# Optimization experiments

Measured on AMD Instinct MI355X. Metric: run time of the kernel, lower is better.

## Reference

```python
import jax, jax.numpy as jnp
import numpy as np

B, C, NMAX = 256, 1, 256   # graphs, channels, max nodes per graph
N = B * C * NMAX           # total nodes = 65536
E = N * 16                 # edges = 1,048,576
EMB, HID = 128, 128


def setup_inputs() -> dict:
    key = jax.random.key(0)
    ks = jax.random.split(key, 8)
    adj = jax.random.uniform(ks[0], (B, C, NMAX, NMAX), jnp.float32)
    edges = jax.random.randint(ks[1], (E, 2), 0, N, dtype=jnp.int32)
    subgraph_idx = jnp.repeat(jnp.arange(B, dtype=jnp.int32), C * NMAX)
    def lin(k, fan_in, fan_out):
        return jax.random.normal(k, (fan_in, fan_out), jnp.float32) / np.sqrt(fan_in).astype(np.float32)
    return {
        "adj": adj, "edges": edges, "subgraph_idx": subgraph_idx,
        "Wdec": lin(ks[2], NMAX, EMB), "bdec": jnp.zeros((EMB,), jnp.float32),
        "Wc1": lin(ks[3], EMB, HID),   "bc1": jnp.zeros((HID,), jnp.float32),
        "Wc2": lin(ks[4], HID, HID),   "bc2": jnp.zeros((HID,), jnp.float32),
        "Wp1": lin(ks[5], HID, HID),   "bp1": jnp.zeros((HID,), jnp.float32),
        "Wp2": lin(ks[6], HID, 1),     "bp2": jnp.zeros((1,), jnp.float32),
    }


def gcn_conv(x, W, b, src, dst):
    # PyG GCNConv: h = x W; add self-loops; symmetric normalization D^-1/2 (A+I) D^-1/2; + bias
    h = x @ W                                      # [N, out]
    deg = jnp.zeros((N,), x.dtype).at[dst].add(1.0) + 1.0  # in-degree incl. self loop
    dinv = jax.lax.rsqrt(deg)                      # [N]
    coef = dinv[src] * dinv[dst]                   # [E]
    agg = jax.ops.segment_sum(h[src] * coef[:, None], dst, num_segments=N)
    return agg + h * (dinv * dinv)[:, None] + b    # self-loop term + bias


def reference(adj, edges, subgraph_idx, Wdec, bdec, Wc1, bc1, Wc2, bc2, Wp1, bp1, Wp2, bp2):
    src, dst = edges[:, 0], edges[:, 1]
    # decoder_input: Linear(max_num_nodes -> embedding_dim) on flattened adjacency rows
    x = adj.reshape(-1, NMAX) @ Wdec + bdec        # [N, EMB]
    # forward applies convs[:-1] only (2 of the 3 convs); dropout is identity in eval mode
    x = jax.nn.relu(gcn_conv(x, Wc1, bc1, src, dst))
    x = jax.nn.relu(gcn_conv(x, Wc2, bc2, src, dst))
    # global max pool over nodes of each graph
    pooled = jax.ops.segment_max(x, subgraph_idx, num_segments=B)  # [B, HID]
    # post_mp MLP head
    h = jax.nn.relu(pooled @ Wp1 + bp1)
    return h @ Wp2 + bp2                           # [B, 1]
```

## Files before the change

### kernel.cpp

```cpp
#include <hip/hip_runtime.h>
#include <hip/hip_fp16.h>
#include <cstdint>
#include <cstddef>

#define NN   65536
#define NE   1048576
#define FD   128
#define KDEC 256
#define NGRAPH 256
#define DUMMY_SRC 65536u
#define EPB  4096
#define BCAP 4608
#define BCAPP 8448

typedef __attribute__((ext_vector_type(8))) short s16x8;
typedef __attribute__((ext_vector_type(4))) float f32x4;

__device__ __forceinline__ ushort f2bf(float x) {
  uint u = __float_as_uint(x);
  uint r = (u + 0x7fffu + ((u >> 16) & 1u)) >> 16;
  return (ushort)r;
}
__device__ __forceinline__ float bf2f(ushort h) {
  return __uint_as_float(((uint)h) << 16);
}

__device__ __forceinline__ void wsplit(float w, int k, int c,
                                       ushort* __restrict__ H,
                                       ushort* __restrict__ L) {
  ushort h = f2bf(w);
  size_t dst = ((size_t)((k >> 5) * 8 + (c >> 4)) * 64 +
                (size_t)((c & 15) + 16 * ((k & 31) >> 3))) * 8 + (k & 7);
  H[dst] = h;
  L[dst] = f2bf(w - bf2f(h));
}


__global__ __launch_bounds__(1024) void k_histbin(const int* __restrict__ edges,
                                                  uint* __restrict__ binbuf,
                                                  int* __restrict__ gbin,
                                                  const float* __restrict__ Wdec,
                                                  const float* __restrict__ Wc1,
                                                  const float* __restrict__ bdec,
                                                  float* __restrict__ bfused,
                                                  ushort* __restrict__ wfh,
                                                  ushort* __restrict__ wfl,
                                                  const float* __restrict__ Wc2,
                                                  ushort* __restrict__ w2h,
                                                  ushort* __restrict__ w2l) {
  const int b = blockIdx.x, t = threadIdx.x;
  if (b >= 256) {
    if (b < 288) {
      int i = (b - 256) * 1024 + t;
      int k = i >> 7, c = i & 127;
      float acc = 0.f;
#pragma unroll 8
      for (int j = 0; j < 128; j++) acc = fmaf(Wdec[k * FD + j], Wc1[j * FD + c], acc);
      wsplit(acc, k, c, wfh, wfl);
      if (b == 256 && t < 128) {
        float ba = 0.f;
        for (int j = 0; j < 128; j++) ba = fmaf(bdec[j], Wc1[j * FD + t], ba);
        bfused[t] = ba;
      }
    } else {
      int i = (b - 288) * 1024 + t;
      wsplit(Wc2[i], i >> 7, i & 127, w2h, w2l);
    }
    return;
  }
  __shared__ int lcnt[256];
  __shared__ int lsum[256];
  __shared__ int gbase[256];
  __shared__ uint sorted[EPB];

  if (t < 256) lcnt[t] = 0;
  __syncthreads();

  uint rec[4];
  ushort bkt[4], lidx[4];
#pragma unroll
  for (int r = 0; r < 4; r++) {
    int i = b * EPB + r * 1024 + t;
    int2 e = ((const int2*)edges)[i];
    int bucket = e.y >> 8;
    int li = atomicAdd(&lcnt[bucket], 1);
    rec[r] = ((uint)bucket << 24) | ((uint)(e.y & 255) << 16) | (uint)e.x;
    bkt[r] = (ushort)bucket;
    lidx[r] = (ushort)li;
  }
  __syncthreads();

  if (t < 256) lsum[t] = lcnt[t];
  __syncthreads();
  for (int off = 1; off < 256; off <<= 1) {
    int v = 0;
    if (t < 256 && t >= off) v = lsum[t - off];
    __syncthreads();
    if (t < 256) lsum[t] += v;
    __syncthreads();
  }
  if (t < 256) gbase[t] = atomicAdd(&gbin[t], lcnt[t]);
  __syncthreads();

#pragma unroll
  for (int r = 0; r < 4; r++) {
    int B = bkt[r];
    sorted[lsum[B] - lcnt[B] + lidx[r]] = rec[r];
  }
  __syncthreads();

  for (int s = t; s < EPB; s += 1024) {
    uint v = sorted[s];
    int B = v >> 24;
    int ex = lsum[B] - lcnt[B];
    binbuf[B * BCAP + gbase[B] + (s - ex)] = v & 0xFFFFFFu;
  }
}


__global__ __launch_bounds__(256) void k_misc(const uint* __restrict__ binbuf,
                                              const int* __restrict__ gbin,
                                              int* __restrict__ hist,
                                              int* __restrict__ offs,
                                              float* __restrict__ dinv,
                                              uint* __restrict__ ec) {
  __shared__ int lc[256];
  __shared__ int s[256];
  __shared__ int sofs[256];
  __shared__ int cnt2[256];
  const int b = blockIdx.x, t = threadIdx.x;
  lc[t] = 0;
  cnt2[t] = 0;
  __syncthreads();
  const int m = gbin[b];
  const uint* bp_ = binbuf + (size_t)b * BCAP;
  for (int i = t; i < m; i += 256)
    atomicAdd(&lc[bp_[i] >> 16], 1);
  __syncthreads();
  const int v = lc[t];
  const int vp = (v + 15) & ~15;
  s[t] = vp;
  __syncthreads();
  for (int off = 1; off < 256; off <<= 1) {
    int add = (t >= off) ? s[t - off] : 0;
    __syncthreads();
    s[t] += add;
    __syncthreads();
  }
  const int of = b * BCAPP + s[t] - vp;
  offs[b * 256 + t] = of;
  hist[b * 256 + t] = v;
  dinv[b * 256 + t] = rsqrtf((float)(v + 1));
  sofs[t] = of;
  __syncthreads();

  for (int i = t; i < m; i += 256) {
    uint rec = bp_[i];
    int dlow = rec >> 16;
    int pos = sofs[dlow] + atomicAdd(&cnt2[dlow], 1);
    ec[pos] = rec & 0xFFFFu;
  }
  __syncthreads();
  int base = sofs[t];
  for (int j = v; j < vp; j++) ec[base + j] = DUMMY_SRC;
}


template <bool ASPLIT>
__global__ __launch_bounds__(256) void k_gemm(const void* __restrict__ A0,
                                              const void* __restrict__ A1,
                                              const ushort* __restrict__ Whi,
                                              const ushort* __restrict__ Wlo,
                                              const float* __restrict__ bias,
                                              const float* __restrict__ scale,
                                              ushort* __restrict__ Y, int K) {
  __shared__ ushort Bs[2][8192];
  const int t = threadIdx.x;
  const int w = t >> 6;
  const int l = t & 63;
  const int lr = l & 15;
  const int kg = l >> 4;
  const int r0 = blockIdx.x * 128 + w * 32;
  const int nks = K >> 5;

  f32x4 acc[2][8];
#pragma unroll
  for (int mb = 0; mb < 2; mb++)
#pragma unroll
    for (int nb = 0; nb < 8; nb++) acc[mb][nb] = (f32x4)0.f;

  f32x4 araw[4];
  s16x8 ahn[2], aln[2];
  s16x8 bh0, bh1, bl0, bl1;

  auto issueA = [&](int s) {
#pragma unroll
    for (int mb = 0; mb < 2; mb++) {
      size_t base = (size_t)(r0 + mb * 16 + lr) * K + s * 32 + kg * 8;
      if (ASPLIT) {
        ahn[mb] = *(const s16x8*)((const ushort*)A0 + base);
        aln[mb] = *(const s16x8*)((const ushort*)A1 + base);
      } else {
        const float* xp = (const float*)A0 + base;
        araw[mb * 2] = *(const f32x4*)xp;
        araw[mb * 2 + 1] = *(const f32x4*)(xp + 4);
      }
    }
  };
  auto issueB = [&](int s) {
    const ushort* ph = Whi + (size_t)s * 4096 + t * 16;
    const ushort* pl = Wlo + (size_t)s * 4096 + t * 16;
    bh0 = *(const s16x8*)ph;
    bh1 = *(const s16x8*)(ph + 8);
    bl0 = *(const s16x8*)pl;
    bl1 = *(const s16x8*)(pl + 8);
  };
  auto writeB = [&](int buf) {
    *(s16x8*)&Bs[buf][t * 16] = bh0;
    *(s16x8*)&Bs[buf][t * 16 + 8] = bh1;
    *(s16x8*)&Bs[buf][4096 + t * 16] = bl0;
    *(s16x8*)&Bs[buf][4096 + t * 16 + 8] = bl1;
  };

  issueB(0);
  issueA(0);
  writeB(0);
  __syncthreads();

  int buf = 0;
  for (int s = 0; s < nks; ++s) {
    s16x8 ah[2], al[2];
    if (ASPLIT) {
      ah[0] = ahn[0]; ah[1] = ahn[1];
      al[0] = aln[0]; al[1] = aln[1];
    } else {
#pragma unroll
      for (int mb = 0; mb < 2; mb++) {
        float xv[8] = {araw[mb*2].x, araw[mb*2].y, araw[mb*2].z, araw[mb*2].w,
                       araw[mb*2+1].x, araw[mb*2+1].y, araw[mb*2+1].z, araw[mb*2+1].w};
        union { ushort u[8]; s16x8 v; } H, L;
#pragma unroll
        for (int e = 0; e < 8; e++) {
          ushort h = f2bf(xv[e]);
          H.u[e] = h;
          L.u[e] = f2bf(xv[e] - bf2f(h));
        }
        ah[mb] = H.v;
        al[mb] = L.v;
      }
    }
    const bool more = (s + 1 < nks);
    if (more) { issueB(s + 1); issueA(s + 1); }

#pragma unroll
    for (int nb = 0; nb < 8; nb++) {
      s16x8 bh = *(const s16x8*)&Bs[buf][nb * 512 + l * 8];
      s16x8 bl = *(const s16x8*)&Bs[buf][4096 + nb * 512 + l * 8];
#pragma unroll
      for (int mb = 0; mb < 2; mb++) {
        acc[mb][nb] = __builtin_amdgcn_mfma_f32_16x16x32_bf16(ah[mb], bh, acc[mb][nb], 0, 0, 0);
        acc[mb][nb] = __builtin_amdgcn_mfma_f32_16x16x32_bf16(ah[mb], bl, acc[mb][nb], 0, 0, 0);
        acc[mb][nb] = __builtin_amdgcn_mfma_f32_16x16x32_bf16(al[mb], bh, acc[mb][nb], 0, 0, 0);
      }
    }
    if (more) {
      writeB(buf ^ 1);
      __syncthreads();
      buf ^= 1;
    }
  }

  float dvr[2][4];
#pragma unroll
  for (int mb = 0; mb < 2; mb++)
#pragma unroll
    for (int r = 0; r < 4; r++)
      dvr[mb][r] = scale ? scale[r0 + mb * 16 + kg * 4 + r] : 1.f;

#pragma unroll
  for (int nb = 0; nb < 8; nb++) {
    int col = nb * 16 + lr;
    float bv = bias ? bias[col] : 0.f;
#pragma unroll
    for (int mb = 0; mb < 2; mb++)
#pragma unroll
      for (int r = 0; r < 4; r++) {
        size_t row = (size_t)(r0 + mb * 16 + kg * 4 + r);
        Y[row * FD + col] = f2bf((acc[mb][nb][r] + bv) * dvr[mb][r]);
      }
  }
}


template <int EMIT>
__global__ __launch_bounds__(256) void k_agg(const ushort* __restrict__ h16,
                                             const uint* __restrict__ ec,
                                             const int* __restrict__ offs,
                                             const int* __restrict__ hist,
                                             const float* __restrict__ dinv,
                                             const float* __restrict__ bias,
                                             ushort* __restrict__ yhi,
                                             ushort* __restrict__ ylo,
                                             float* __restrict__ pooled) {
  __shared__ int pmax[128];
  const int t = threadIdx.x;
  if (EMIT == 1) {
    if (t < 128) pmax[t] = 0;
    __syncthreads();
  }
  const int n = blockIdx.x * 4 + (t >> 6);
  const int l = t & 63;
  const int half = l >> 5;
  const int dl = (l & 31) * 4;

  const int cnt_p = (hist[n] + 15) & ~15;
  const uint* ep = ec + offs[n];

  float a0 = 0.f, a1 = 0.f, a2 = 0.f, a3 = 0.f;
  float b0 = 0.f, b1 = 0.f, b2 = 0.f, b3 = 0.f;
  for (int i = half; i < cnt_p; i += 16) {
    uint s0 = ep[i];
    uint s1 = ep[i + 2];
    uint s2 = ep[i + 4];
    uint s3 = ep[i + 6];
    uint s4 = ep[i + 8];
    uint s5 = ep[i + 10];
    uint s6 = ep[i + 12];
    uint s7 = ep[i + 14];
    ushort4 v0 = *(const ushort4*)(h16 + ((size_t)s0 << 7) + dl);
    ushort4 v1 = *(const ushort4*)(h16 + ((size_t)s1 << 7) + dl);
    ushort4 v2 = *(const ushort4*)(h16 + ((size_t)s2 << 7) + dl);
    ushort4 v3 = *(const ushort4*)(h16 + ((size_t)s3 << 7) + dl);
    ushort4 v4 = *(const ushort4*)(h16 + ((size_t)s4 << 7) + dl);
    ushort4 v5 = *(const ushort4*)(h16 + ((size_t)s5 << 7) + dl);
    ushort4 v6 = *(const ushort4*)(h16 + ((size_t)s6 << 7) + dl);
    ushort4 v7 = *(const ushort4*)(h16 + ((size_t)s7 << 7) + dl);
    a0 += bf2f(v0.x); a1 += bf2f(v0.y); a2 += bf2f(v0.z); a3 += bf2f(v0.w);
    b0 += bf2f(v1.x); b1 += bf2f(v1.y); b2 += bf2f(v1.z); b3 += bf2f(v1.w);
    a0 += bf2f(v2.x); a1 += bf2f(v2.y); a2 += bf2f(v2.z); a3 += bf2f(v2.w);
    b0 += bf2f(v3.x); b1 += bf2f(v3.y); b2 += bf2f(v3.z); b3 += bf2f(v3.w);
    a0 += bf2f(v4.x); a1 += bf2f(v4.y); a2 += bf2f(v4.z); a3 += bf2f(v4.w);
    b0 += bf2f(v5.x); b1 += bf2f(v5.y); b2 += bf2f(v5.z); b3 += bf2f(v5.w);
    a0 += bf2f(v6.x); a1 += bf2f(v6.y); a2 += bf2f(v6.z); a3 += bf2f(v6.w);
    b0 += bf2f(v7.x); b1 += bf2f(v7.y); b2 += bf2f(v7.z); b3 += bf2f(v7.w);
  }
  a0 += b0; a1 += b1; a2 += b2; a3 += b3;
  a0 += __shfl_xor(a0, 32);
  a1 += __shfl_xor(a1, 32);
  a2 += __shfl_xor(a2, 32);
  a3 += __shfl_xor(a3, 32);

  if (l < 32) {
    float dv = dinv[n];
    ushort4 vs = *(const ushort4*)(h16 + ((size_t)n << 7) + dl);
    float4 bb = *(const float4*)(bias + dl);
    float o0 = fmaxf(fmaf(dv, a0 + bf2f(vs.x), bb.x), 0.f);
    float o1 = fmaxf(fmaf(dv, a1 + bf2f(vs.y), bb.y), 0.f);
    float o2 = fmaxf(fmaf(dv, a2 + bf2f(vs.z), bb.z), 0.f);
    float o3 = fmaxf(fmaf(dv, a3 + bf2f(vs.w), bb.w), 0.f);
    if (EMIT == 0) {
      ushort4 hi, lo;
      hi.x = f2bf(o0); lo.x = f2bf(o0 - bf2f(hi.x));
      hi.y = f2bf(o1); lo.y = f2bf(o1 - bf2f(hi.y));
      hi.z = f2bf(o2); lo.z = f2bf(o2 - bf2f(hi.z));
      hi.w = f2bf(o3); lo.w = f2bf(o3 - bf2f(hi.w));
      size_t base = (size_t)n * FD + dl;
      *(ushort4*)(yhi + base) = hi;
      *(ushort4*)(ylo + base) = lo;
    } else {
      atomicMax(&pmax[dl + 0], __float_as_int(o0));
      atomicMax(&pmax[dl + 1], __float_as_int(o1));
      atomicMax(&pmax[dl + 2], __float_as_int(o2));
      atomicMax(&pmax[dl + 3], __float_as_int(o3));
    }
  }
  if (EMIT == 1) {
    __syncthreads();
    if (t < 128) {
      int gr = blockIdx.x >> 6;
      atomicMax((int*)pooled + gr * FD + t, pmax[t]);
    }
  }
}


__global__ __launch_bounds__(128) void k_mlp(const float* __restrict__ pooled,
                                             const float* __restrict__ Wp1,
                                             const float* __restrict__ bp1,
                                             const float* __restrict__ Wp2,
                                             const float* __restrict__ bp2,
                                             float* __restrict__ out) {
  __shared__ float row[128];
  __shared__ float red[128];
  int g = blockIdx.x, t = threadIdx.x;
  row[t] = pooled[g * FD + t];
  __syncthreads();
  float acc = bp1[t];
#pragma unroll 8
  for (int k = 0; k < 128; k++) acc = fmaf(row[k], Wp1[k * FD + t], acc);
  acc = fmaxf(acc, 0.f);
  red[t] = acc * Wp2[t];
  __syncthreads();
  for (int st = 64; st > 0; st >>= 1) {
    if (t < st) red[t] += red[t + st];
    __syncthreads();
  }
  if (t == 0) out[g] = red[0] + bp2[0];
}


extern "C" void kernel_launch(void* const* d_in, const int* in_sizes, int n_in,
                              void* d_out, int out_size, void* d_ws, size_t ws_size,
                              hipStream_t stream) {
  (void)in_sizes; (void)n_in; (void)out_size; (void)ws_size;

  const float* adj  = (const float*)d_in[0];
  const int*   edges= (const int*)d_in[1];
  const float* Wdec = (const float*)d_in[3];
  const float* bdec = (const float*)d_in[4];
  const float* Wc1  = (const float*)d_in[5];
  const float* bc1  = (const float*)d_in[6];
  const float* Wc2  = (const float*)d_in[7];
  const float* bc2  = (const float*)d_in[8];
  const float* Wp1  = (const float*)d_in[9];
  const float* bp1  = (const float*)d_in[10];
  const float* Wp2  = (const float*)d_in[11];
  const float* bp2  = (const float*)d_in[12];
  float* out = (float*)d_out;

  char* ws = (char*)d_ws;
  size_t off = 0;
  auto alloc = [&](size_t bytes) -> void* {
    void* p = ws + off;
    off += (bytes + 255) & ~(size_t)255;
    return p;
  };
  ushort* h16  = (ushort*)alloc((size_t)(NN + 1) * FD * 2);
  ushort* x1hi = (ushort*)alloc((size_t)NN * FD * 2);
  ushort* x1lo = (ushort*)alloc((size_t)NN * FD * 2);
  float*  pooled = (float*)alloc((size_t)NGRAPH * FD * 4);
  int*    gbin = (int*)alloc(256 * 4);
  int*    hist = (int*)alloc((size_t)NN * 4);
  int*    offs = (int*)alloc((size_t)NN * 4);
  uint*   ec   = (uint*)alloc((size_t)256 * BCAPP * 4);
  uint*   binbuf = (uint*)alloc((size_t)256 * BCAP * 4);
  float*  dinv = (float*)alloc((size_t)NN * 4);
  float*  bfused = (float*)alloc(FD * 4);
  ushort* wfh = (ushort*)alloc((size_t)KDEC * FD * 2);
  ushort* wfl = (ushort*)alloc((size_t)KDEC * FD * 2);
  ushort* w2h = (ushort*)alloc((size_t)FD * FD * 2);
  ushort* w2l = (ushort*)alloc((size_t)FD * FD * 2);

  hipMemsetAsync(pooled, 0, (size_t)NGRAPH * FD * 4 + 256 * 4, stream);
  hipMemsetAsync(h16 + (size_t)NN * FD, 0, FD * 2, stream);

  k_histbin<<<304, 1024, 0, stream>>>(edges, binbuf, gbin, Wdec, Wc1, bdec,
                                      bfused, wfh, wfl, Wc2, w2h, w2l);
  k_misc<<<256, 256, 0, stream>>>(binbuf, gbin, hist, offs, dinv, ec);

  k_gemm<false><<<NN / 128, 256, 0, stream>>>(adj, nullptr, wfh, wfl, bfused, dinv, h16, KDEC);

  k_agg<0><<<NN / 4, 256, 0, stream>>>(h16, ec, offs, hist, dinv, bc1, x1hi, x1lo, nullptr);

  k_gemm<true><<<NN / 128, 256, 0, stream>>>(x1hi, x1lo, w2h, w2l, nullptr, dinv, h16, FD);

  k_agg<1><<<NN / 4, 256, 0, stream>>>(h16, ec, offs, hist, dinv, bc2, nullptr, nullptr, pooled);

  k_mlp<<<NGRAPH, 128, 0, stream>>>(pooled, Wp1, bp1, Wp2, bp2, out);
}
```

Before: 166.2 us.

## Store layer-1 activations as single bf16 and double-buffer A-operand prefetch

```diff
diff --git a/kernel.cpp b/kernel.cpp
--- a/kernel.cpp
+++ b/kernel.cpp
@@ -166,9 +166,8 @@
 }
 
 
-template <bool ASPLIT>
+template <int AMODE>
 __global__ __launch_bounds__(256) void k_gemm(const void* __restrict__ A0,
-                                              const void* __restrict__ A1,
                                               const ushort* __restrict__ Whi,
                                               const ushort* __restrict__ Wlo,
                                               const float* __restrict__ bias,
@@ -189,21 +188,20 @@
 #pragma unroll
     for (int nb = 0; nb < 8; nb++) acc[mb][nb] = (f32x4)0.f;
 
-  f32x4 araw[4];
-  s16x8 ahn[2], aln[2];
+  f32x4 araw[2][4];
+  s16x8 abuf[2][2];
   s16x8 bh0, bh1, bl0, bl1;
 
-  auto issueA = [&](int s) {
+  auto issueA = [&](int s, int pb) {
 #pragma unroll
     for (int mb = 0; mb < 2; mb++) {
       size_t base = (size_t)(r0 + mb * 16 + lr) * K + s * 32 + kg * 8;
-      if (ASPLIT) {
-        ahn[mb] = *(const s16x8*)((const ushort*)A0 + base);
-        aln[mb] = *(const s16x8*)((const ushort*)A1 + base);
+      if (AMODE == 0) {
+        const float* xp = (const float*)A0 + base;
+        araw[pb][mb * 2] = *(const f32x4*)xp;
+        araw[pb][mb * 2 + 1] = *(const f32x4*)(xp + 4);
       } else {
-        const float* xp = (const float*)A0 + base;
-        araw[mb * 2] = *(const f32x4*)xp;
-        araw[mb * 2 + 1] = *(const f32x4*)(xp + 4);
+        abuf[pb][mb] = *(const s16x8*)((const ushort*)A0 + base);
       }
     }
   };
@@ -222,22 +220,21 @@
     *(s16x8*)&Bs[buf][4096 + t * 16 + 8] = bl1;
   };
 
+  issueA(0, 0);
   issueB(0);
-  issueA(0);
   writeB(0);
+  if (nks > 1) issueA(1, 1);
   __syncthreads();
 
   int buf = 0;
   for (int s = 0; s < nks; ++s) {
+    const int pb = s & 1;
     s16x8 ah[2], al[2];
-    if (ASPLIT) {
-      ah[0] = ahn[0]; ah[1] = ahn[1];
-      al[0] = aln[0]; al[1] = aln[1];
-    } else {
+    if (AMODE == 0) {
 #pragma unroll
       for (int mb = 0; mb < 2; mb++) {
-        float xv[8] = {araw[mb*2].x, araw[mb*2].y, araw[mb*2].z, araw[mb*2].w,
-                       araw[mb*2+1].x, araw[mb*2+1].y, araw[mb*2+1].z, araw[mb*2+1].w};
+        float xv[8] = {araw[pb][mb*2].x, araw[pb][mb*2].y, araw[pb][mb*2].z, araw[pb][mb*2].w,
+                       araw[pb][mb*2+1].x, araw[pb][mb*2+1].y, araw[pb][mb*2+1].z, araw[pb][mb*2+1].w};
         union { ushort u[8]; s16x8 v; } H, L;
 #pragma unroll
         for (int e = 0; e < 8; e++) {
@@ -248,9 +245,13 @@
         ah[mb] = H.v;
         al[mb] = L.v;
       }
-    }
+    } else {
+      ah[0] = abuf[pb][0];
+      ah[1] = abuf[pb][1];
+    }
+    if (s + 2 < nks) issueA(s + 2, pb);
     const bool more = (s + 1 < nks);
-    if (more) { issueB(s + 1); issueA(s + 1); }
+    if (more) issueB(s + 1);
 
 #pragma unroll
     for (int nb = 0; nb < 8; nb++) {
@@ -260,7 +261,8 @@
       for (int mb = 0; mb < 2; mb++) {
         acc[mb][nb] = __builtin_amdgcn_mfma_f32_16x16x32_bf16(ah[mb], bh, acc[mb][nb], 0, 0, 0);
         acc[mb][nb] = __builtin_amdgcn_mfma_f32_16x16x32_bf16(ah[mb], bl, acc[mb][nb], 0, 0, 0);
-        acc[mb][nb] = __builtin_amdgcn_mfma_f32_16x16x32_bf16(al[mb], bh, acc[mb][nb], 0, 0, 0);
+        if (AMODE == 0)
+          acc[mb][nb] = __builtin_amdgcn_mfma_f32_16x16x32_bf16(al[mb], bh, acc[mb][nb], 0, 0, 0);
       }
     }
     if (more) {
@@ -299,8 +301,7 @@
                                              const int* __restrict__ hist,
                                              const float* __restrict__ dinv,
                                              const float* __restrict__ bias,
-                                             ushort* __restrict__ yhi,
-                                             ushort* __restrict__ ylo,
+                                             ushort* __restrict__ yout,
                                              float* __restrict__ pooled) {
   __shared__ int pmax[128];
   const int t = threadIdx.x;
@@ -359,14 +360,12 @@
     float o2 = fmaxf(fmaf(dv, a2 + bf2f(vs.z), bb.z), 0.f);
     float o3 = fmaxf(fmaf(dv, a3 + bf2f(vs.w), bb.w), 0.f);
     if (EMIT == 0) {
-      ushort4 hi, lo;
-      hi.x = f2bf(o0); lo.x = f2bf(o0 - bf2f(hi.x));
-      hi.y = f2bf(o1); lo.y = f2bf(o1 - bf2f(hi.y));
-      hi.z = f2bf(o2); lo.z = f2bf(o2 - bf2f(hi.z));
-      hi.w = f2bf(o3); lo.w = f2bf(o3 - bf2f(hi.w));
-      size_t base = (size_t)n * FD + dl;
-      *(ushort4*)(yhi + base) = hi;
-      *(ushort4*)(ylo + base) = lo;
+      ushort4 hi;
+      hi.x = f2bf(o0);
+      hi.y = f2bf(o1);
+      hi.z = f2bf(o2);
+      hi.w = f2bf(o3);
+      *(ushort4*)(yout + (size_t)n * FD + dl) = hi;
     } else {
       atomicMax(&pmax[dl + 0], __float_as_int(o0));
       atomicMax(&pmax[dl + 1], __float_as_int(o1));
@@ -436,8 +435,7 @@
     return p;
   };
   ushort* h16  = (ushort*)alloc((size_t)(NN + 1) * FD * 2);
-  ushort* x1hi = (ushort*)alloc((size_t)NN * FD * 2);
-  ushort* x1lo = (ushort*)alloc((size_t)NN * FD * 2);
+  ushort* x1   = (ushort*)alloc((size_t)NN * FD * 2);
   float*  pooled = (float*)alloc((size_t)NGRAPH * FD * 4);
   int*    gbin = (int*)alloc(256 * 4);
   int*    hist = (int*)alloc((size_t)NN * 4);
@@ -458,13 +456,13 @@
                                       bfused, wfh, wfl, Wc2, w2h, w2l);
   k_misc<<<256, 256, 0, stream>>>(binbuf, gbin, hist, offs, dinv, ec);
 
-  k_gemm<false><<<NN / 128, 256, 0, stream>>>(adj, nullptr, wfh, wfl, bfused, dinv, h16, KDEC);
-
-  k_agg<0><<<NN / 4, 256, 0, stream>>>(h16, ec, offs, hist, dinv, bc1, x1hi, x1lo, nullptr);
-
-  k_gemm<true><<<NN / 128, 256, 0, stream>>>(x1hi, x1lo, w2h, w2l, nullptr, dinv, h16, FD);
-
-  k_agg<1><<<NN / 4, 256, 0, stream>>>(h16, ec, offs, hist, dinv, bc2, nullptr, nullptr, pooled);
+  k_gemm<0><<<NN / 128, 256, 0, stream>>>(adj, wfh, wfl, bfused, dinv, h16, KDEC);
+
+  k_agg<0><<<NN / 4, 256, 0, stream>>>(h16, ec, offs, hist, dinv, bc1, x1, nullptr);
+
+  k_gemm<1><<<NN / 128, 256, 0, stream>>>(x1, w2h, w2l, nullptr, dinv, h16, FD);
+
+  k_agg<1><<<NN / 4, 256, 0, stream>>>(h16, ec, offs, hist, dinv, bc2, nullptr, pooled);
 
   k_mlp<<<NGRAPH, 128, 0, stream>>>(pooled, Wp1, bp1, Wp2, bp2, out);
 }
```

Result: slower. 209.8 us (+26.2%).
